# Optimization experiments

Hardware: AMD Instinct MI355X
Metric: run time of the kernel (lower is better)

The kernel has to match this reference:

```python
import jax, jax.numpy as jnp
import numpy as np

NUM_RAYS = 262144   # 512x512 rays
LENGTH = 128        # path_length
NUM_LEAVES = 1048576
MAX_DIST = 1e10
EPS = 1e-10


def setup_inputs() -> dict:
    key = jax.random.key(0)
    k1, k2, k3 = jax.random.split(key, 3)
    # t_stops must be increasing along each ray
    t_stops = jnp.sort(jax.random.uniform(k1, (NUM_RAYS, LENGTH), jnp.float32, 0.0, 4.0), axis=-1)
    leaves = jax.random.randint(k2, (NUM_RAYS, LENGTH), 0, NUM_LEAVES, dtype=jnp.int64)
    logits = jax.random.normal(k3, (NUM_LEAVES,), jnp.float32) - 10.0  # init near -10 like the module
    return {"t_stops": t_stops, "leaves": leaves, "logits": logits}


def reference(t_stops, leaves, logits):
    num_rays, length = leaves.shape
    # gather per-sample opacity
    opacity = jax.nn.sigmoid(logits)[leaves]                      # [R, L]
    # segment lengths; last segment extends to "infinity"
    deltas = jnp.concatenate(
        [t_stops[:, 1:] - t_stops[:, :-1],
         jnp.full((num_rays, 1), MAX_DIST, dtype=t_stops.dtype)], axis=-1)
    alpha = 1.0 - jnp.exp(-(opacity * deltas))                    # [R, L]
    trans = jnp.minimum(1.0, 1.0 - alpha + EPS)
    # shift right: transmittance before first sample is 1
    trans = jnp.concatenate(
        [jnp.ones((num_rays, 1), dtype=alpha.dtype), trans[:, 1:]], axis=-1)
    weights = alpha * jnp.cumprod(trans, axis=-1)                 # [R, L]
    return weights.sum(axis=-1)                                   # [R]
```

## Files before the change

kernel.cpp:

```cpp
#include <hip/hip_runtime.h>
#include <hip/hip_fp16.h>
#include <math.h>


#define NRAYS 262144
#define LEN   128
#define NLEAF 1048576
#define MAXD  1e10f
#define EPSW  1e-10f

typedef float v4f __attribute__((ext_vector_type(4)));
typedef int   v4i __attribute__((ext_vector_type(4)));

__device__ __forceinline__ float fast_sigmoid(float x) {
    return __builtin_amdgcn_rcpf(1.0f + __expf(-x));
}

__device__ __forceinline__ float omexp(float x) {
    float p = x * (1.0f + x * (-0.5f + x * (0.16666667f - 0.041666668f * x)));
    return (x < 0.1f) ? p : (1.0f - __expf(-x));
}

__device__ __forceinline__ float tab_gather(const unsigned short* tb, int idx) {
    unsigned short u = __hip_atomic_load(tb + idx, __ATOMIC_RELAXED,
                                         __HIP_MEMORY_SCOPE_AGENT);
    __half h;
    *(unsigned short*)&h = u;
    return __half2float(h);
}

__global__ __launch_bounds__(256) void sig_kernel(const float* __restrict__ logits,
                                                  __half* __restrict__ tab) {
    int i = blockIdx.x * 256 + threadIdx.x;
    tab[i] = __float2half(fast_sigmoid(logits[i]));
}

template <bool TAB>
__global__ __launch_bounds__(256) void vc_kernel(
    const float* __restrict__ t_stops,
    const int*   __restrict__ leaves,
    const void*  __restrict__ table,
    float*       __restrict__ out)
{
    const int lane = threadIdx.x & 63;
    const int wid  = blockIdx.x * 4 + (threadIdx.x >> 6);
    const int ray  = wid * 4 + (lane >> 4);
    const int sub  = lane & 15;

    const long long b0 = (long long)ray * LEN + sub * 4;
    const long long b1 = b0 + 64;

    v4i l0 = __builtin_nontemporal_load((const v4i*)(leaves + b0));
    v4i l1 = __builtin_nontemporal_load((const v4i*)(leaves + b1));
    v4f t0 = __builtin_nontemporal_load((const v4f*)(t_stops + b0));
    v4f t1 = __builtin_nontemporal_load((const v4f*)(t_stops + b1));

    float op0, op1, op2, op3, op4, op5, op6, op7;
    if (TAB) {
        const unsigned short* tb = (const unsigned short*)table;
        op0 = tab_gather(tb, l0.x);  op1 = tab_gather(tb, l0.y);
        op2 = tab_gather(tb, l0.z);  op3 = tab_gather(tb, l0.w);
        op4 = tab_gather(tb, l1.x);  op5 = tab_gather(tb, l1.y);
        op6 = tab_gather(tb, l1.z);  op7 = tab_gather(tb, l1.w);
    } else {
        const float* lg = (const float*)table;
        op0 = fast_sigmoid(lg[l0.x]);  op1 = fast_sigmoid(lg[l0.y]);
        op2 = fast_sigmoid(lg[l0.z]);  op3 = fast_sigmoid(lg[l0.w]);
        op4 = fast_sigmoid(lg[l1.x]);  op5 = fast_sigmoid(lg[l1.y]);
        op6 = fast_sigmoid(lg[l1.z]);  op7 = fast_sigmoid(lg[l1.w]);
    }

    float tn0  = __shfl_down(t0.x, 1);
    float tn1  = __shfl_down(t1.x, 1);
    float tb1x = __shfl(t1.x, lane & 48);

    float d0a = t0.y - t0.x, d0b = t0.z - t0.y, d0c = t0.w - t0.z;
    float d0d = (sub == 15) ? (tb1x - t0.w) : (tn0 - t0.w);
    float d1a = t1.y - t1.x, d1b = t1.z - t1.y, d1c = t1.w - t1.z;
    float d1d = (sub == 15) ? MAXD : (tn1 - t1.w);

    float a0 = omexp(op0 * d0a), a1 = omexp(op1 * d0b);
    float a2 = omexp(op2 * d0c), a3 = omexp(op3 * d0d);
    float a4 = omexp(op4 * d1a), a5 = omexp(op5 * d1b);
    float a6 = omexp(op6 * d1c), a7 = omexp(op7 * d1d);

    float r0 = fminf(1.0f, 1.0f - a0 + EPSW), r1 = fminf(1.0f, 1.0f - a1 + EPSW);
    float r2 = fminf(1.0f, 1.0f - a2 + EPSW), r3 = fminf(1.0f, 1.0f - a3 + EPSW);
    float r4 = fminf(1.0f, 1.0f - a4 + EPSW), r5 = fminf(1.0f, 1.0f - a5 + EPSW);
    float r6 = fminf(1.0f, 1.0f - a6 + EPSW), r7 = fminf(1.0f, 1.0f - a7 + EPSW);
    if (sub == 0) r0 = 1.0f;

    float c0 = r0;            float S0 = a0 * c0;
    c0 *= r1;                 S0 = fmaf(a1, c0, S0);
    c0 *= r2;                 S0 = fmaf(a2, c0, S0);
    c0 *= r3;                 S0 = fmaf(a3, c0, S0);
    float P0 = c0;
    float c1 = r4;            float S1 = a4 * c1;
    c1 *= r5;                 S1 = fmaf(a5, c1, S1);
    c1 *= r6;                 S1 = fmaf(a6, c1, S1);
    c1 *= r7;                 S1 = fmaf(a7, c1, S1);
    float P1 = c1;

    #pragma unroll
    for (int o = 1; o < 16; o <<= 1) {
        float Pp0 = __shfl_xor(P0, o), Sp0 = __shfl_xor(S0, o);
        float Pp1 = __shfl_xor(P1, o), Sp1 = __shfl_xor(S1, o);
        if (lane & o) {
            S0 = fmaf(Pp0, S0, Sp0);
            S1 = fmaf(Pp1, S1, Sp1);
        } else {
            S0 = fmaf(P0, Sp0, S0);
            S1 = fmaf(P1, Sp1, S1);
        }
        P0 *= Pp0;
        P1 *= Pp1;
    }

    float S = fmaf(P0, S1, S0);
    if (sub == 0)
        out[ray] = S;
}

extern "C" void kernel_launch(void* const* d_in, const int* in_sizes, int n_in,
                              void* d_out, int out_size, void* d_ws, size_t ws_size,
                              hipStream_t stream) {
    const float* t_stops = (const float*)d_in[0];
    const int*   leaves  = (const int*)d_in[1];
    const float* logits  = (const float*)d_in[2];
    float*       out     = (float*)d_out;

    if (ws_size >= NLEAF * sizeof(__half)) {
        sig_kernel<<<NLEAF / 256, 256, 0, stream>>>(logits, (__half*)d_ws);
        vc_kernel<true><<<NRAYS / 16, 256, 0, stream>>>(t_stops, leaves, d_ws, out);
    } else {
        vc_kernel<false><<<NRAYS / 16, 256, 0, stream>>>(t_stops, leaves, logits, out);
    }
}
```

Measured before the change: 371.5 us.

## Process 8 rays per wave with 16 samples per lane and 32-bit table gathers

Each lane now handles 16 samples in four chunks, so each 8-lane group covers one ray and the grid is halved. This cuts scan shuffle rounds from four to three per chunk and raises memory-level parallelism per thread. The fp16 sigmoid table is now read as aligned 32-bit words with a shift, replacing 16-bit atomic loads. The cost is more registers per thread and a serial fold across the four chunks.

```diff
diff --git a/kernel.cpp b/kernel.cpp
--- a/kernel.cpp
+++ b/kernel.cpp
@@ -21,9 +21,9 @@
     return (x < 0.1f) ? p : (1.0f - __expf(-x));
 }
 
-__device__ __forceinline__ float tab_gather(const unsigned short* tb, int idx) {
-    unsigned short u = __hip_atomic_load(tb + idx, __ATOMIC_RELAXED,
-                                         __HIP_MEMORY_SCOPE_AGENT);
+__device__ __forceinline__ float tab_gather32(const unsigned int* tb32, int idx) {
+    unsigned int v = tb32[idx >> 1];
+    unsigned short u = (unsigned short)(v >> ((idx & 1) * 16));
     __half h;
     *(unsigned short*)&h = u;
     return __half2float(h);
@@ -44,81 +44,89 @@
 {
     const int lane = threadIdx.x & 63;
     const int wid  = blockIdx.x * 4 + (threadIdx.x >> 6);
-    const int ray  = wid * 4 + (lane >> 4);
-    const int sub  = lane & 15;
+    const int ray  = wid * 8 + (lane >> 3);
+    const int sub  = lane & 7;
+    const int gbase = lane & 56;
 
-    const long long b0 = (long long)ray * LEN + sub * 4;
-    const long long b1 = b0 + 64;
+    const long long rb = (long long)ray * LEN + sub * 4;
 
-    v4i l0 = __builtin_nontemporal_load((const v4i*)(leaves + b0));
-    v4i l1 = __builtin_nontemporal_load((const v4i*)(leaves + b1));
-    v4f t0 = __builtin_nontemporal_load((const v4f*)(t_stops + b0));
-    v4f t1 = __builtin_nontemporal_load((const v4f*)(t_stops + b1));
+    v4i lv[4];
+    v4f tt[4];
+    #pragma unroll
+    for (int c = 0; c < 4; ++c)
+        lv[c] = __builtin_nontemporal_load((const v4i*)(leaves + rb + c * 32));
+    #pragma unroll
+    for (int c = 0; c < 4; ++c)
+        tt[c] = __builtin_nontemporal_load((const v4f*)(t_stops + rb + c * 32));
 
-    float op0, op1, op2, op3, op4, op5, op6, op7;
+    float op[4][4];
     if (TAB) {
-        const unsigned short* tb = (const unsigned short*)table;
-        op0 = tab_gather(tb, l0.x);  op1 = tab_gather(tb, l0.y);
-        op2 = tab_gather(tb, l0.z);  op3 = tab_gather(tb, l0.w);
-        op4 = tab_gather(tb, l1.x);  op5 = tab_gather(tb, l1.y);
-        op6 = tab_gather(tb, l1.z);  op7 = tab_gather(tb, l1.w);
+        const unsigned int* tb32 = (const unsigned int*)table;
+        #pragma unroll
+        for (int c = 0; c < 4; ++c) {
+            op[c][0] = tab_gather32(tb32, lv[c].x);
+            op[c][1] = tab_gather32(tb32, lv[c].y);
+            op[c][2] = tab_gather32(tb32, lv[c].z);
+            op[c][3] = tab_gather32(tb32, lv[c].w);
+        }
     } else {
         const float* lg = (const float*)table;
-        op0 = fast_sigmoid(lg[l0.x]);  op1 = fast_sigmoid(lg[l0.y]);
-        op2 = fast_sigmoid(lg[l0.z]);  op3 = fast_sigmoid(lg[l0.w]);
-        op4 = fast_sigmoid(lg[l1.x]);  op5 = fast_sigmoid(lg[l1.y]);
-        op6 = fast_sigmoid(lg[l1.z]);  op7 = fast_sigmoid(lg[l1.w]);
+        #pragma unroll
+        for (int c = 0; c < 4; ++c) {
+            op[c][0] = fast_sigmoid(lg[lv[c].x]);
+            op[c][1] = fast_sigmoid(lg[lv[c].y]);
+            op[c][2] = fast_sigmoid(lg[lv[c].z]);
+            op[c][3] = fast_sigmoid(lg[lv[c].w]);
+        }
     }
 
-    float tn0  = __shfl_down(t0.x, 1);
-    float tn1  = __shfl_down(t1.x, 1);
-    float tb1x = __shfl(t1.x, lane & 48);
+    float P[4], S[4];
+    #pragma unroll
+    for (int c = 0; c < 4; ++c) {
+        float nxt_dn = __shfl_down(tt[c].x, 1);
+        float nxt_c1 = (c < 3) ? __shfl(tt[(c + 1) & 3].x, gbase) : MAXD;
+        float nxt = (sub == 7) ? nxt_c1 : nxt_dn;
 
-    float d0a = t0.y - t0.x, d0b = t0.z - t0.y, d0c = t0.w - t0.z;
-    float d0d = (sub == 15) ? (tb1x - t0.w) : (tn0 - t0.w);
-    float d1a = t1.y - t1.x, d1b = t1.z - t1.y, d1c = t1.w - t1.z;
-    float d1d = (sub == 15) ? MAXD : (tn1 - t1.w);
+        float d0 = tt[c].y - tt[c].x;
+        float d1 = tt[c].z - tt[c].y;
+        float d2 = tt[c].w - tt[c].z;
+        float d3 = nxt - tt[c].w;
 
-    float a0 = omexp(op0 * d0a), a1 = omexp(op1 * d0b);
-    float a2 = omexp(op2 * d0c), a3 = omexp(op3 * d0d);
-    float a4 = omexp(op4 * d1a), a5 = omexp(op5 * d1b);
-    float a6 = omexp(op6 * d1c), a7 = omexp(op7 * d1d);
+        float a0 = omexp(op[c][0] * d0);
+        float a1 = omexp(op[c][1] * d1);
+        float a2 = omexp(op[c][2] * d2);
+        float a3 = omexp(op[c][3] * d3);
 
-    float r0 = fminf(1.0f, 1.0f - a0 + EPSW), r1 = fminf(1.0f, 1.0f - a1 + EPSW);
-    float r2 = fminf(1.0f, 1.0f - a2 + EPSW), r3 = fminf(1.0f, 1.0f - a3 + EPSW);
-    float r4 = fminf(1.0f, 1.0f - a4 + EPSW), r5 = fminf(1.0f, 1.0f - a5 + EPSW);
-    float r6 = fminf(1.0f, 1.0f - a6 + EPSW), r7 = fminf(1.0f, 1.0f - a7 + EPSW);
-    if (sub == 0) r0 = 1.0f;
+        float r0 = fminf(1.0f, 1.0f - a0 + EPSW);
+        float r1 = fminf(1.0f, 1.0f - a1 + EPSW);
+        float r2 = fminf(1.0f, 1.0f - a2 + EPSW);
+        float r3 = fminf(1.0f, 1.0f - a3 + EPSW);
+        if (c == 0 && sub == 0) r0 = 1.0f;
 
-    float c0 = r0;            float S0 = a0 * c0;
-    c0 *= r1;                 S0 = fmaf(a1, c0, S0);
-    c0 *= r2;                 S0 = fmaf(a2, c0, S0);
-    c0 *= r3;                 S0 = fmaf(a3, c0, S0);
-    float P0 = c0;
-    float c1 = r4;            float S1 = a4 * c1;
-    c1 *= r5;                 S1 = fmaf(a5, c1, S1);
-    c1 *= r6;                 S1 = fmaf(a6, c1, S1);
-    c1 *= r7;                 S1 = fmaf(a7, c1, S1);
-    float P1 = c1;
+        float cc = r0;        float ss = a0 * cc;
+        cc *= r1;             ss = fmaf(a1, cc, ss);
+        cc *= r2;             ss = fmaf(a2, cc, ss);
+        cc *= r3;             ss = fmaf(a3, cc, ss);
+        P[c] = cc;  S[c] = ss;
+    }
 
     #pragma unroll
-    for (int o = 1; o < 16; o <<= 1) {
-        float Pp0 = __shfl_xor(P0, o), Sp0 = __shfl_xor(S0, o);
-        float Pp1 = __shfl_xor(P1, o), Sp1 = __shfl_xor(S1, o);
-        if (lane & o) {
-            S0 = fmaf(Pp0, S0, Sp0);
-            S1 = fmaf(Pp1, S1, Sp1);
-        } else {
-            S0 = fmaf(P0, Sp0, S0);
-            S1 = fmaf(P1, Sp1, S1);
+    for (int o = 1; o < 8; o <<= 1) {
+        #pragma unroll
+        for (int c = 0; c < 4; ++c) {
+            float Pp = __shfl_xor(P[c], o);
+            float Sp = __shfl_xor(S[c], o);
+            S[c] = (lane & o) ? fmaf(Pp, S[c], Sp) : fmaf(P[c], Sp, S[c]);
+            P[c] *= Pp;
         }
-        P0 *= Pp0;
-        P1 *= Pp1;
     }
 
-    float S = fmaf(P0, S1, S0);
+    float Sr = fmaf(P[2], S[3], S[2]);
+    Sr = fmaf(P[1], Sr, S[1]);
+    Sr = fmaf(P[0], Sr, S[0]);
+
     if (sub == 0)
-        out[ray] = S;
+        out[ray] = Sr;
 }
 
 extern "C" void kernel_launch(void* const* d_in, const int* in_sizes, int n_in,
@@ -131,8 +139,8 @@
 
     if (ws_size >= NLEAF * sizeof(__half)) {
         sig_kernel<<<NLEAF / 256, 256, 0, stream>>>(logits, (__half*)d_ws);
-        vc_kernel<true><<<NRAYS / 16, 256, 0, stream>>>(t_stops, leaves, d_ws, out);
+        vc_kernel<true><<<NRAYS / 32, 256, 0, stream>>>(t_stops, leaves, d_ws, out);
     } else {
-        vc_kernel<false><<<NRAYS / 16, 256, 0, stream>>>(t_stops, leaves, logits, out);
+        vc_kernel<false><<<NRAYS / 32, 256, 0, stream>>>(t_stops, leaves, logits, out);
     }
 }
```

New measurement: 366.2 us (median of 2 runs). No clear change (-1.4%).
